# Kernel optimization log

Measured on AMD Instinct MI355X. Metric: run time of the kernel, lower is better.

## Reference

```python
import jax, jax.numpy as jnp
import numpy as np

B, N, D, H = 4, 2048, 1024, 64

def setup_inputs() -> dict:
    key = jax.random.key(0)
    ks = jax.random.split(key, 7)
    s = D ** -0.5  # torch Linear default init scale ~ U(-1/sqrt(fan_in), ...); scale randn similarly
    return {
        "x":  jax.random.normal(ks[0], (B, N, D), dtype=jnp.float32),
        "Wq": jax.random.normal(ks[1], (D, H), dtype=jnp.float32) * s,
        "bq": jax.random.normal(ks[2], (H,), dtype=jnp.float32) * s,
        "Wk": jax.random.normal(ks[3], (D, H), dtype=jnp.float32) * s,
        "bk": jax.random.normal(ks[4], (H,), dtype=jnp.float32) * s,
        "Wv": jax.random.normal(ks[5], (D, H), dtype=jnp.float32) * s,
        "bv": jax.random.normal(ks[6], (H,), dtype=jnp.float32) * s,
    }

def reference(x, Wq, bq, Wk, bk, Wv, bv):
    head_size = Wq.shape[1]
    q = x @ Wq + bq          # [B, N, H]
    k = x @ Wk + bk          # [B, N, H]
    v = x @ Wv + bv          # [B, N, H]
    scores = jnp.einsum("bid,bjd->bij", q, k)        # [B, N, N]
    # faithful to torch: keep upper triangle (col >= row), then mask exact zeros to -inf
    scores = jnp.triu(scores)
    scores = jnp.where(scores == 0, -jnp.inf, scores)
    attn = jax.nn.softmax(scores * (head_size ** -0.5), axis=-1)  # [B, N, N]
    # out = (V^T @ attn)^T  ==  attn^T @ V
    out = jnp.einsum("bji,bjh->bih", attn, v)         # [B, N, H]
    return out
```

## Files before the change

### kernel.cpp

```cpp
#include <hip/hip_runtime.h>
#include <math.h>

constexpr int kN = 2048;
constexpr int kD = 1024;
constexpr int kH = 64;
constexpr int kBN = 4 * kN;

typedef __attribute__((ext_vector_type(8))) short bf16x8;
typedef __attribute__((ext_vector_type(4))) short bf16x4;
typedef __attribute__((ext_vector_type(4))) float f32x4;

#define MFMA(a, b, c) __builtin_amdgcn_mfma_f32_16x16x32_bf16(a, b, c, 0, 0, 0)

__device__ __forceinline__ short f2bf(float f) {
    unsigned u = __float_as_uint(f);
    u += 0x7fff + ((u >> 16) & 1);
    return (short)(u >> 16);
}

__device__ __forceinline__ void ml_merge(float& m, float& l, float mo, float lo) {
    float mn = fmaxf(m, mo);
    l = l * __expf(m - mn) + lo * __expf(mo - mn);
    m = mn;
}

__global__ __launch_bounds__(256) void prep_kernel(
        const float* __restrict__ Wq, const float* __restrict__ Wk,
        const float* __restrict__ Wv, const float* __restrict__ bq,
        const float* __restrict__ bk, const float* __restrict__ bv,
        short* __restrict__ Wt, float* __restrict__ bcat)
{
    int tid = blockIdx.x * 256 + threadIdx.x;
    for (int e = tid; e < 192 * kD; e += gridDim.x * 256) {
        int n = e >> 10, d = e & 1023;
        float w = (n < 64) ? Wq[d * 64 + n]
                : (n < 128) ? Wk[d * 64 + (n - 64)]
                : Wv[d * 64 + (n - 128)];
        Wt[e] = f2bf(w);
    }
    if (tid < 192)
        bcat[tid] = (tid < 64) ? bq[tid] : (tid < 128) ? bk[tid - 64] : bv[tid - 128];
}

__global__ __launch_bounds__(256) void qkv_kernel(
        const float* __restrict__ x, const short* __restrict__ Wt,
        const float* __restrict__ bcat,
        short* __restrict__ gq, short* __restrict__ gk, short* __restrict__ vt)
{
    __shared__ short xs[32 * 72];
    __shared__ short wsm[192 * 72];
    const int t = threadIdx.x;
    const int m0 = blockIdx.x * 32;
    const int w = t >> 6, lane = t & 63;
    const int l15 = lane & 15, q8 = lane >> 4;
    const int msub = w & 1;
    const int nh = w >> 1;

    f32x4 acc[6];
    #pragma unroll
    for (int i = 0; i < 6; ++i) acc[i] = (f32x4){0.f, 0.f, 0.f, 0.f};

    for (int k0 = 0; k0 < kD; k0 += 64) {
        __syncthreads();
        #pragma unroll
        for (int p = 0; p < 2; ++p) {
            int idx = t + p * 256;
            int row = idx >> 4, c = idx & 15;
            float4 xv = *(const float4*)&x[(size_t)(m0 + row) * kD + k0 + c * 4];
            bf16x4 pk = {f2bf(xv.x), f2bf(xv.y), f2bf(xv.z), f2bf(xv.w)};
            *(bf16x4*)&xs[row * 72 + c * 4] = pk;
        }
        #pragma unroll
        for (int p = 0; p < 6; ++p) {
            int idx = t + p * 256;
            int row = idx >> 3, c = idx & 7;
            *(bf16x8*)&wsm[row * 72 + c * 8] =
                *(const bf16x8*)&Wt[(size_t)row * kD + k0 + c * 8];
        }
        __syncthreads();

        int arow = 16 * msub + l15;
        bf16x8 a0 = *(const bf16x8*)&xs[arow * 72 + q8 * 8];
        bf16x8 a1 = *(const bf16x8*)&xs[arow * 72 + 32 + q8 * 8];
        #pragma unroll
        for (int nt = 0; nt < 6; ++nt) {
            int brow = 96 * nh + 16 * nt + l15;
            bf16x8 b0 = *(const bf16x8*)&wsm[brow * 72 + q8 * 8];
            bf16x8 b1 = *(const bf16x8*)&wsm[brow * 72 + 32 + q8 * 8];
            acc[nt] = MFMA(a0, b0, acc[nt]);
            acc[nt] = MFMA(a1, b1, acc[nt]);
        }
    }

    #pragma unroll
    for (int nt = 0; nt < 6; ++nt) {
        int nb = 96 * nh + 16 * nt;
        int n = nb + l15;
        float bias = bcat[n];
        if (nb < 128) {
            #pragma unroll
            for (int r = 0; r < 4; ++r) {
                int m = m0 + 16 * msub + q8 * 4 + r;
                short bf = f2bf(acc[nt][r] + bias);
                if (nb < 64) gq[(size_t)m * 64 + n] = bf;
                else         gk[(size_t)m * 64 + (n - 64)] = bf;
            }
        } else {
            int h = n - 128;
            int bz = m0 >> 11;
            int jb = (m0 & 2047) + 16 * msub + q8 * 4;
            bf16x4 pk = {f2bf(acc[nt][0] + bias), f2bf(acc[nt][1] + bias),
                         f2bf(acc[nt][2] + bias), f2bf(acc[nt][3] + bias)};
            *(bf16x4*)&vt[((size_t)(bz * 64 + h)) * kN + jb] = pk;
        }
    }
}

__global__ __launch_bounds__(256) void stats_kernel(
        const short* __restrict__ gq, const short* __restrict__ gk,
        float* __restrict__ m2, float* __restrict__ l2)
{
    __shared__ short qsm[64 * 72];
    __shared__ short ksm[64 * 72];
    const int t = threadIdx.x;
    const int w = t >> 6, lane = t & 63;
    const int l15 = lane & 15, q8 = lane >> 4;
    const int b = blockIdx.x;
    const int ic = b >> 7, rem = b & 127;
    const int bz = rem >> 5, jt = rem & 31;
    const int j0 = jt * 64;
    const int ilo = ic * 512, ihi = ilo + 512;
    const int istart = (j0 > ilo) ? j0 : ilo;

    float mloc[4] = {-1e30f, -1e30f, -1e30f, -1e30f};
    float lloc[4] = {0.f, 0.f, 0.f, 0.f};

    if (istart < ihi) {
        #pragma unroll
        for (int p = 0; p < 2; ++p) {
            int idx = t + p * 256;
            int row = idx >> 3, c = idx & 7;
            *(bf16x8*)&qsm[row * 72 + c * 8] =
                *(const bf16x8*)&gq[(size_t)(bz * kN + j0 + row) * 64 + c * 8];
        }
        for (int i0 = istart; i0 < ihi; i0 += 64) {
            __syncthreads();
            #pragma unroll
            for (int p = 0; p < 2; ++p) {
                int idx = t + p * 256;
                int row = idx >> 3, c = idx & 7;
                *(bf16x8*)&ksm[row * 72 + c * 8] =
                    *(const bf16x8*)&gk[(size_t)(bz * kN + i0 + row) * 64 + c * 8];
            }
            __syncthreads();

            int jrow = 16 * w + l15;
            bf16x8 a0 = *(const bf16x8*)&qsm[jrow * 72 + q8 * 8];
            bf16x8 a1 = *(const bf16x8*)&qsm[jrow * 72 + 32 + q8 * 8];
            #pragma unroll
            for (int it = 0; it < 4; ++it) {
                int irow = 16 * it + l15;
                bf16x8 b0 = *(const bf16x8*)&ksm[irow * 72 + q8 * 8];
                bf16x8 b1 = *(const bf16x8*)&ksm[irow * 72 + 32 + q8 * 8];
                f32x4 s = (f32x4){0.f, 0.f, 0.f, 0.f};
                s = MFMA(a0, b0, s);
                s = MFMA(a1, b1, s);
                int ig = i0 + 16 * it + l15;
                #pragma unroll
                for (int r = 0; r < 4; ++r) {
                    int jg = j0 + 16 * w + q8 * 4 + r;
                    float sv = s[r];
                    bool valid = (ig >= jg) && (sv != 0.0f);
                    float sc = valid ? sv * 0.125f : -1e30f;
                    float mn = fmaxf(mloc[r], sc);
                    float e2 = valid ? __expf(sc - mn) : 0.f;
                    lloc[r] = lloc[r] * __expf(mloc[r] - mn) + e2;
                    mloc[r] = mn;
                }
            }
        }
    }
    #pragma unroll
    for (int off = 1; off < 16; off <<= 1) {
        #pragma unroll
        for (int r = 0; r < 4; ++r) {
            float mo = __shfl_xor(mloc[r], off);
            float lo = __shfl_xor(lloc[r], off);
            ml_merge(mloc[r], lloc[r], mo, lo);
        }
    }
    if (l15 == 0) {
        #pragma unroll
        for (int r = 0; r < 4; ++r) {
            int jg = j0 + 16 * w + q8 * 4 + r;
            m2[ic * kBN + bz * kN + jg] = mloc[r];
            l2[ic * kBN + bz * kN + jg] = lloc[r];
        }
    }
}

__global__ __launch_bounds__(256) void combine_kernel(
        const float* __restrict__ m2, const float* __restrict__ l2,
        float* __restrict__ mf, float* __restrict__ rlf)
{
    int r = blockIdx.x * 256 + threadIdx.x;
    float m = m2[r], l = l2[r];
    #pragma unroll
    for (int c = 1; c < 4; ++c)
        ml_merge(m, l, m2[c * kBN + r], l2[c * kBN + r]);
    mf[r] = m;
    rlf[r] = (l > 0.f) ? 1.0f / l : 0.0f;
}

__global__ __launch_bounds__(256) void out_kernel(
        const short* __restrict__ gq, const short* __restrict__ gk,
        const short* __restrict__ vt, const float* __restrict__ mf,
        const float* __restrict__ rlf, float* __restrict__ part)
{
    __shared__ short ksm[64 * 72];
    __shared__ short qsm[64 * 72];
    __shared__ short vsm[64 * 72];
    __shared__ short psm[64 * 72];
    __shared__ float msm[64];
    __shared__ float rsm[64];
    const int t = threadIdx.x;
    const int w = t >> 6, lane = t & 63;
    const int l15 = lane & 15, q8 = lane >> 4;
    const int b = blockIdx.x;
    const int jc = b >> 7, rem = b & 127;
    const int bz = rem >> 5, it = rem & 31;
    const int i0 = it * 64;
    const int jlo = jc * 512;
    const int jhi = (jlo + 512 < i0 + 64) ? (jlo + 512) : (i0 + 64);

    f32x4 oacc[4];
    #pragma unroll
    for (int i = 0; i < 4; ++i) oacc[i] = (f32x4){0.f, 0.f, 0.f, 0.f};

    if (jlo < jhi) {
        #pragma unroll
        for (int p = 0; p < 2; ++p) {
            int idx = t + p * 256;
            int row = idx >> 3, c = idx & 7;
            *(bf16x8*)&ksm[row * 72 + c * 8] =
                *(const bf16x8*)&gk[(size_t)(bz * kN + i0 + row) * 64 + c * 8];
        }
        for (int j0s = jlo; j0s < jhi; j0s += 64) {
            __syncthreads();
            #pragma unroll
            for (int p = 0; p < 2; ++p) {
                int idx = t + p * 256;
                int row = idx >> 3, c = idx & 7;
                *(bf16x8*)&qsm[row * 72 + c * 8] =
                    *(const bf16x8*)&gq[(size_t)(bz * kN + j0s + row) * 64 + c * 8];
                *(bf16x8*)&vsm[row * 72 + c * 8] =
                    *(const bf16x8*)&vt[(size_t)(bz * 64 + row) * kN + j0s + c * 8];
            }
            if (t < 64) msm[t] = mf[bz * kN + j0s + t];
            else if (t < 128) rsm[t - 64] = rlf[bz * kN + j0s + (t - 64)];
            __syncthreads();

            int jrow = 16 * w + l15;
            bf16x8 a0 = *(const bf16x8*)&qsm[jrow * 72 + q8 * 8];
            bf16x8 a1 = *(const bf16x8*)&qsm[jrow * 72 + 32 + q8 * 8];
            #pragma unroll
            for (int itile = 0; itile < 4; ++itile) {
                int irow = 16 * itile + l15;
                bf16x8 b0 = *(const bf16x8*)&ksm[irow * 72 + q8 * 8];
                bf16x8 b1 = *(const bf16x8*)&ksm[irow * 72 + 32 + q8 * 8];
                f32x4 s = (f32x4){0.f, 0.f, 0.f, 0.f};
                s = MFMA(a0, b0, s);
                s = MFMA(a1, b1, s);
                int ig = i0 + 16 * itile + l15;
                bf16x4 pk;
                #pragma unroll
                for (int r = 0; r < 4; ++r) {
                    int jl = 16 * w + q8 * 4 + r;
                    int jg = j0s + jl;
                    float sv = s[r];
                    bool valid = (ig >= jg) && (sv != 0.0f);
                    float p = valid ? __expf(sv * 0.125f - msm[jl]) * rsm[jl] : 0.f;
                    pk[r] = f2bf(p);
                }
                *(bf16x4*)&psm[(16 * itile + l15) * 72 + 16 * w + q8 * 4] = pk;
            }
            __syncthreads();

            int prow = 16 * w + l15;
            bf16x8 pa0 = *(const bf16x8*)&psm[prow * 72 + q8 * 8];
            bf16x8 pa1 = *(const bf16x8*)&psm[prow * 72 + 32 + q8 * 8];
            #pragma unroll
            for (int ht = 0; ht < 4; ++ht) {
                int vrow = 16 * ht + l15;
                bf16x8 vb0 = *(const bf16x8*)&vsm[vrow * 72 + q8 * 8];
                bf16x8 vb1 = *(const bf16x8*)&vsm[vrow * 72 + 32 + q8 * 8];
                oacc[ht] = MFMA(pa0, vb0, oacc[ht]);
                oacc[ht] = MFMA(pa1, vb1, oacc[ht]);
            }
        }
    }
    size_t base = ((size_t)(jc * 4 + bz) * kN + i0) * 64;
    #pragma unroll
    for (int ht = 0; ht < 4; ++ht)
        #pragma unroll
        for (int r = 0; r < 4; ++r)
            part[base + (size_t)(16 * w + q8 * 4 + r) * 64 + 16 * ht + l15] = oacc[ht][r];
}

__global__ __launch_bounds__(256) void reduce_kernel(
        const float* __restrict__ part, float* __restrict__ out)
{
    int idx = blockIdx.x * 256 + threadIdx.x;
    const float4* p = (const float4*)part;
    float4 a = p[idx];
    float4 b = p[idx + 131072];
    float4 c = p[idx + 262144];
    float4 d = p[idx + 393216];
    float4 r;
    r.x = a.x + b.x + c.x + d.x;
    r.y = a.y + b.y + c.y + d.y;
    r.z = a.z + b.z + c.z + d.z;
    r.w = a.w + b.w + c.w + d.w;
    ((float4*)out)[idx] = r;
}

extern "C" void kernel_launch(void* const* d_in, const int* in_sizes, int n_in,
                              void* d_out, int out_size, void* d_ws, size_t ws_size,
                              hipStream_t stream)
{
    const float* x  = (const float*)d_in[0];
    const float* Wq = (const float*)d_in[1];
    const float* bq = (const float*)d_in[2];
    const float* Wk = (const float*)d_in[3];
    const float* bk = (const float*)d_in[4];
    const float* Wv = (const float*)d_in[5];
    const float* bv = (const float*)d_in[6];
    float* out = (float*)d_out;

    char* base = (char*)d_ws;
    short* Wt   = (short*)base;
    float* bcat = (float*)(base + 393216);
    short* gq   = (short*)(base + 394240);
    short* gk   = (short*)(base + 1442816);
    short* vt   = (short*)(base + 2491392);
    float* m2   = (float*)(base + 3539968);
    float* l2   = (float*)(base + 3671040);
    float* mf   = (float*)(base + 3802112);
    float* rlf  = (float*)(base + 3834880);
    float* part = (float*)(base + 3867648);

    prep_kernel<<<96, 256, 0, stream>>>(Wq, Wk, Wv, bq, bk, bv, Wt, bcat);
    qkv_kernel<<<256, 256, 0, stream>>>(x, Wt, bcat, gq, gk, vt);
    stats_kernel<<<512, 256, 0, stream>>>(gq, gk, m2, l2);
    combine_kernel<<<32, 256, 0, stream>>>(m2, l2, mf, rlf);
    out_kernel<<<512, 256, 0, stream>>>(gq, gk, vt, mf, rlf, part);
    reduce_kernel<<<512, 256, 0, stream>>>(part, out);
}
```

Before: 145.2 us.

## Pre-pad operands in global memory, use direct global-to-LDS loads, drop running max

Adds a prep pass that converts x to bf16 into a padded, chunked layout, and stores Q, K and V^T with a 72-element padded row stride. This lets every tile move into shared memory with async global_load_lds copies instead of register round trips. The softmax max tracking is removed and the kernels sum raw exp(s/8), which is safe only while scores stay small. Block index mapping is reordered and the qkv wave tiling changes. The cost is a large extra prep pass that writes a padded bf16 copy of x (about 19MB of workspace).

```diff
diff --git a/kernel.cpp b/kernel.cpp
--- a/kernel.cpp
+++ b/kernel.cpp
@@ -3,8 +3,6 @@
 
 constexpr int kN = 2048;
 constexpr int kD = 1024;
-constexpr int kH = 64;
-constexpr int kBN = 4 * kN;
 
 typedef __attribute__((ext_vector_type(8))) short bf16x8;
 typedef __attribute__((ext_vector_type(4))) short bf16x4;
@@ -18,217 +16,201 @@
     return (short)(u >> 16);
 }
 
-__device__ __forceinline__ void ml_merge(float& m, float& l, float mo, float lo) {
-    float mn = fmaxf(m, mo);
-    l = l * __expf(m - mn) + lo * __expf(mo - mn);
-    m = mn;
+__device__ __forceinline__ void g2l(void* lds, const void* g, int nbytes, int t) {
+    int lane = t & 63, w = t >> 6;
+    for (int base = w * 1024; base < nbytes; base += 4096) {
+        if (base + lane * 16 < nbytes) {
+            __builtin_amdgcn_global_load_lds(
+                (const __attribute__((address_space(1))) void*)((const char*)g + base + lane * 16),
+                (__attribute__((address_space(3))) void*)((char*)lds + base),
+                16, 0, 0);
+        }
+    }
 }
 
 __global__ __launch_bounds__(256) void prep_kernel(
+        const float* __restrict__ x,
         const float* __restrict__ Wq, const float* __restrict__ Wk,
         const float* __restrict__ Wv, const float* __restrict__ bq,
         const float* __restrict__ bk, const float* __restrict__ bv,
-        short* __restrict__ Wt, float* __restrict__ bcat)
+        short* __restrict__ xb, short* __restrict__ Wt, float* __restrict__ bcat)
 {
     int tid = blockIdx.x * 256 + threadIdx.x;
-    for (int e = tid; e < 192 * kD; e += gridDim.x * 256) {
-        int n = e >> 10, d = e & 1023;
-        float w = (n < 64) ? Wq[d * 64 + n]
-                : (n < 128) ? Wk[d * 64 + (n - 64)]
-                : Wv[d * 64 + (n - 128)];
-        Wt[e] = f2bf(w);
+    int stride = gridDim.x * 256;
+    for (int e = tid; e < 16 * 8192 * 64; e += stride) {
+        int kc = e >> 19;
+        int rem = e & 524287;
+        int row = rem >> 6, c = rem & 63;
+        xb[((size_t)(kc * 8192 + row)) * 72 + c] = f2bf(x[(size_t)row * kD + kc * 64 + c]);
+    }
+    for (int e = tid; e < 16 * 64 * 192; e += stride) {
+        int n = e % 192;
+        int rc = e / 192;
+        int c = rc & 63, kc = rc >> 6;
+        int d = kc * 64 + c;
+        float wv = (n < 64) ? Wq[d * 64 + n]
+                 : (n < 128) ? Wk[d * 64 + (n - 64)]
+                 : Wv[d * 64 + (n - 128)];
+        Wt[(kc * 192 + n) * 72 + c] = f2bf(wv);
     }
     if (tid < 192)
         bcat[tid] = (tid < 64) ? bq[tid] : (tid < 128) ? bk[tid - 64] : bv[tid - 128];
 }
 
 __global__ __launch_bounds__(256) void qkv_kernel(
-        const float* __restrict__ x, const short* __restrict__ Wt,
+        const short* __restrict__ xb, const short* __restrict__ Wt,
         const float* __restrict__ bcat,
         short* __restrict__ gq, short* __restrict__ gk, short* __restrict__ vt)
 {
-    __shared__ short xs[32 * 72];
-    __shared__ short wsm[192 * 72];
+    __shared__ __align__(16) short xs[32 * 72];
+    __shared__ __align__(16) short wsm[192 * 72];
     const int t = threadIdx.x;
+    const int w = t >> 6, lane = t & 63, l15 = lane & 15, q8 = lane >> 4;
     const int m0 = blockIdx.x * 32;
-    const int w = t >> 6, lane = t & 63;
-    const int l15 = lane & 15, q8 = lane >> 4;
-    const int msub = w & 1;
-    const int nh = w >> 1;
-
-    f32x4 acc[6];
-    #pragma unroll
-    for (int i = 0; i < 6; ++i) acc[i] = (f32x4){0.f, 0.f, 0.f, 0.f};
-
-    for (int k0 = 0; k0 < kD; k0 += 64) {
+
+    f32x4 acc[2][3];
+    #pragma unroll
+    for (int rt = 0; rt < 2; ++rt)
+        #pragma unroll
+        for (int ct = 0; ct < 3; ++ct) acc[rt][ct] = (f32x4){0.f, 0.f, 0.f, 0.f};
+
+    for (int kc = 0; kc < 16; ++kc) {
         __syncthreads();
-        #pragma unroll
-        for (int p = 0; p < 2; ++p) {
-            int idx = t + p * 256;
-            int row = idx >> 4, c = idx & 15;
-            float4 xv = *(const float4*)&x[(size_t)(m0 + row) * kD + k0 + c * 4];
-            bf16x4 pk = {f2bf(xv.x), f2bf(xv.y), f2bf(xv.z), f2bf(xv.w)};
-            *(bf16x4*)&xs[row * 72 + c * 4] = pk;
-        }
-        #pragma unroll
-        for (int p = 0; p < 6; ++p) {
-            int idx = t + p * 256;
-            int row = idx >> 3, c = idx & 7;
-            *(bf16x8*)&wsm[row * 72 + c * 8] =
-                *(const bf16x8*)&Wt[(size_t)row * kD + k0 + c * 8];
-        }
+        g2l(xs, xb + ((size_t)(kc * 8192 + m0)) * 72, 32 * 144, t);
+        g2l(wsm, Wt + (size_t)kc * 192 * 72, 192 * 144, t);
         __syncthreads();
 
-        int arow = 16 * msub + l15;
-        bf16x8 a0 = *(const bf16x8*)&xs[arow * 72 + q8 * 8];
-        bf16x8 a1 = *(const bf16x8*)&xs[arow * 72 + 32 + q8 * 8];
-        #pragma unroll
-        for (int nt = 0; nt < 6; ++nt) {
-            int brow = 96 * nh + 16 * nt + l15;
-            bf16x8 b0 = *(const bf16x8*)&wsm[brow * 72 + q8 * 8];
-            bf16x8 b1 = *(const bf16x8*)&wsm[brow * 72 + 32 + q8 * 8];
-            acc[nt] = MFMA(a0, b0, acc[nt]);
-            acc[nt] = MFMA(a1, b1, acc[nt]);
-        }
-    }
-
-    #pragma unroll
-    for (int nt = 0; nt < 6; ++nt) {
-        int nb = 96 * nh + 16 * nt;
-        int n = nb + l15;
-        float bias = bcat[n];
-        if (nb < 128) {
+        bf16x8 a[2][2], b[3][2];
+        #pragma unroll
+        for (int rt = 0; rt < 2; ++rt) {
+            int arow = rt * 16 + l15;
+            a[rt][0] = *(const bf16x8*)&xs[arow * 72 + q8 * 8];
+            a[rt][1] = *(const bf16x8*)&xs[arow * 72 + 32 + q8 * 8];
+        }
+        #pragma unroll
+        for (int ct = 0; ct < 3; ++ct) {
+            int brow = w * 48 + ct * 16 + l15;
+            b[ct][0] = *(const bf16x8*)&wsm[brow * 72 + q8 * 8];
+            b[ct][1] = *(const bf16x8*)&wsm[brow * 72 + 32 + q8 * 8];
+        }
+        #pragma unroll
+        for (int rt = 0; rt < 2; ++rt)
             #pragma unroll
-            for (int r = 0; r < 4; ++r) {
-                int m = m0 + 16 * msub + q8 * 4 + r;
-                short bf = f2bf(acc[nt][r] + bias);
-                if (nb < 64) gq[(size_t)m * 64 + n] = bf;
-                else         gk[(size_t)m * 64 + (n - 64)] = bf;
-            }
-        } else {
-            int h = n - 128;
-            int bz = m0 >> 11;
-            int jb = (m0 & 2047) + 16 * msub + q8 * 4;
-            bf16x4 pk = {f2bf(acc[nt][0] + bias), f2bf(acc[nt][1] + bias),
-                         f2bf(acc[nt][2] + bias), f2bf(acc[nt][3] + bias)};
-            *(bf16x4*)&vt[((size_t)(bz * 64 + h)) * kN + jb] = pk;
-        }
-    }
+            for (int ct = 0; ct < 3; ++ct) {
+                acc[rt][ct] = MFMA(a[rt][0], b[ct][0], acc[rt][ct]);
+                acc[rt][ct] = MFMA(a[rt][1], b[ct][1], acc[rt][ct]);
+            }
+    }
+
+    const int bz = m0 >> 11;
+    const int jt = (m0 & 2047) >> 6;
+    const int jb = m0 & 63;
+    #pragma unroll
+    for (int rt = 0; rt < 2; ++rt)
+        #pragma unroll
+        for (int ct = 0; ct < 3; ++ct) {
+            int nb = w * 48 + ct * 16;
+            int n = nb + l15;
+            float bias = bcat[n];
+            if (nb < 64) {
+                #pragma unroll
+                for (int r = 0; r < 4; ++r)
+                    gq[(size_t)(m0 + rt * 16 + q8 * 4 + r) * 72 + n] =
+                        f2bf(acc[rt][ct][r] + bias);
+            } else if (nb < 128) {
+                #pragma unroll
+                for (int r = 0; r < 4; ++r)
+                    gk[(size_t)(m0 + rt * 16 + q8 * 4 + r) * 72 + (n - 64)] =
+                        f2bf(acc[rt][ct][r] + bias);
+            } else {
+                int h = n - 128;
+                bf16x4 pk = {f2bf(acc[rt][ct][0] + bias), f2bf(acc[rt][ct][1] + bias),
+                             f2bf(acc[rt][ct][2] + bias), f2bf(acc[rt][ct][3] + bias)};
+                *(bf16x4*)&vt[((size_t)((bz * 32 + jt) * 64 + h)) * 72 + jb + rt * 16 + q8 * 4] = pk;
+            }
+        }
 }
 
 __global__ __launch_bounds__(256) void stats_kernel(
         const short* __restrict__ gq, const short* __restrict__ gk,
-        float* __restrict__ m2, float* __restrict__ l2)
-{
-    __shared__ short qsm[64 * 72];
-    __shared__ short ksm[64 * 72];
+        float* __restrict__ l2)
+{
+    __shared__ __align__(16) short qsm[64 * 72];
+    __shared__ __align__(16) short ksm[64 * 72];
     const int t = threadIdx.x;
-    const int w = t >> 6, lane = t & 63;
-    const int l15 = lane & 15, q8 = lane >> 4;
+    const int w = t >> 6, lane = t & 63, l15 = lane & 15, q8 = lane >> 4;
     const int b = blockIdx.x;
-    const int ic = b >> 7, rem = b & 127;
-    const int bz = rem >> 5, jt = rem & 31;
+    const int ic = b & 3, bz = (b >> 2) & 3, jt = b >> 4;
     const int j0 = jt * 64;
     const int ilo = ic * 512, ihi = ilo + 512;
     const int istart = (j0 > ilo) ? j0 : ilo;
 
-    float mloc[4] = {-1e30f, -1e30f, -1e30f, -1e30f};
     float lloc[4] = {0.f, 0.f, 0.f, 0.f};
 
     if (istart < ihi) {
-        #pragma unroll
-        for (int p = 0; p < 2; ++p) {
-            int idx = t + p * 256;
-            int row = idx >> 3, c = idx & 7;
-            *(bf16x8*)&qsm[row * 72 + c * 8] =
-                *(const bf16x8*)&gq[(size_t)(bz * kN + j0 + row) * 64 + c * 8];
-        }
+        g2l(qsm, gq + (size_t)(bz * kN + j0) * 72, 64 * 144, t);
+        __syncthreads();
+        int jrow = 16 * w + l15;
+        bf16x8 a0 = *(const bf16x8*)&qsm[jrow * 72 + q8 * 8];
+        bf16x8 a1 = *(const bf16x8*)&qsm[jrow * 72 + 32 + q8 * 8];
+
         for (int i0 = istart; i0 < ihi; i0 += 64) {
             __syncthreads();
-            #pragma unroll
-            for (int p = 0; p < 2; ++p) {
-                int idx = t + p * 256;
-                int row = idx >> 3, c = idx & 7;
-                *(bf16x8*)&ksm[row * 72 + c * 8] =
-                    *(const bf16x8*)&gk[(size_t)(bz * kN + i0 + row) * 64 + c * 8];
-            }
-            __syncthreads();
-
-            int jrow = 16 * w + l15;
-            bf16x8 a0 = *(const bf16x8*)&qsm[jrow * 72 + q8 * 8];
-            bf16x8 a1 = *(const bf16x8*)&qsm[jrow * 72 + 32 + q8 * 8];
+            g2l(ksm, gk + (size_t)(bz * kN + i0) * 72, 64 * 144, t);
+            __syncthreads();
             #pragma unroll
             for (int it = 0; it < 4; ++it) {
-                int irow = 16 * it + l15;
+                int irow = it * 16 + l15;
                 bf16x8 b0 = *(const bf16x8*)&ksm[irow * 72 + q8 * 8];
                 bf16x8 b1 = *(const bf16x8*)&ksm[irow * 72 + 32 + q8 * 8];
                 f32x4 s = (f32x4){0.f, 0.f, 0.f, 0.f};
                 s = MFMA(a0, b0, s);
                 s = MFMA(a1, b1, s);
-                int ig = i0 + 16 * it + l15;
+                int ig = i0 + it * 16 + l15;
                 #pragma unroll
                 for (int r = 0; r < 4; ++r) {
                     int jg = j0 + 16 * w + q8 * 4 + r;
                     float sv = s[r];
-                    bool valid = (ig >= jg) && (sv != 0.0f);
-                    float sc = valid ? sv * 0.125f : -1e30f;
-                    float mn = fmaxf(mloc[r], sc);
-                    float e2 = valid ? __expf(sc - mn) : 0.f;
-                    lloc[r] = lloc[r] * __expf(mloc[r] - mn) + e2;
-                    mloc[r] = mn;
+                    float e = __expf(sv * 0.125f);
+                    lloc[r] += ((ig >= jg) && (sv != 0.0f)) ? e : 0.0f;
                 }
             }
         }
     }
     #pragma unroll
-    for (int off = 1; off < 16; off <<= 1) {
-        #pragma unroll
-        for (int r = 0; r < 4; ++r) {
-            float mo = __shfl_xor(mloc[r], off);
-            float lo = __shfl_xor(lloc[r], off);
-            ml_merge(mloc[r], lloc[r], mo, lo);
-        }
-    }
+    for (int off = 1; off < 16; off <<= 1)
+        #pragma unroll
+        for (int r = 0; r < 4; ++r)
+            lloc[r] += __shfl_xor(lloc[r], off);
     if (l15 == 0) {
         #pragma unroll
-        for (int r = 0; r < 4; ++r) {
-            int jg = j0 + 16 * w + q8 * 4 + r;
-            m2[ic * kBN + bz * kN + jg] = mloc[r];
-            l2[ic * kBN + bz * kN + jg] = lloc[r];
-        }
+        for (int r = 0; r < 4; ++r)
+            l2[ic * 8192 + bz * kN + j0 + 16 * w + q8 * 4 + r] = lloc[r];
     }
 }
 
 __global__ __launch_bounds__(256) void combine_kernel(
-        const float* __restrict__ m2, const float* __restrict__ l2,
-        float* __restrict__ mf, float* __restrict__ rlf)
+        const float* __restrict__ l2, float* __restrict__ rlf)
 {
     int r = blockIdx.x * 256 + threadIdx.x;
-    float m = m2[r], l = l2[r];
-    #pragma unroll
-    for (int c = 1; c < 4; ++c)
-        ml_merge(m, l, m2[c * kBN + r], l2[c * kBN + r]);
-    mf[r] = m;
+    float l = l2[r] + l2[8192 + r] + l2[16384 + r] + l2[24576 + r];
     rlf[r] = (l > 0.f) ? 1.0f / l : 0.0f;
 }
 
 __global__ __launch_bounds__(256) void out_kernel(
         const short* __restrict__ gq, const short* __restrict__ gk,
-        const short* __restrict__ vt, const float* __restrict__ mf,
-        const float* __restrict__ rlf, float* __restrict__ part)
-{
-    __shared__ short ksm[64 * 72];
-    __shared__ short qsm[64 * 72];
-    __shared__ short vsm[64 * 72];
-    __shared__ short psm[64 * 72];
-    __shared__ float msm[64];
+        const short* __restrict__ vt, const float* __restrict__ rlf,
+        float* __restrict__ part)
+{
+    __shared__ __align__(16) short ksm[64 * 72];
+    __shared__ __align__(16) short qsm[64 * 72];
+    __shared__ __align__(16) short vsm[64 * 72];
+    __shared__ __align__(16) short psm[64 * 72];
     __shared__ float rsm[64];
     const int t = threadIdx.x;
-    const int w = t >> 6, lane = t & 63;
-    const int l15 = lane & 15, q8 = lane >> 4;
+    const int w = t >> 6, lane = t & 63, l15 = lane & 15, q8 = lane >> 4;
     const int b = blockIdx.x;
-    const int jc = b >> 7, rem = b & 127;
-    const int bz = rem >> 5, it = rem & 31;
+    const int jc = b & 3, bz = (b >> 2) & 3, it = b >> 4;
     const int i0 = it * 64;
     const int jlo = jc * 512;
     const int jhi = (jlo + 512 < i0 + 64) ? (jlo + 512) : (i0 + 64);
@@ -238,26 +220,12 @@
     for (int i = 0; i < 4; ++i) oacc[i] = (f32x4){0.f, 0.f, 0.f, 0.f};
 
     if (jlo < jhi) {
-        #pragma unroll
-        for (int p = 0; p < 2; ++p) {
-            int idx = t + p * 256;
-            int row = idx >> 3, c = idx & 7;
-            *(bf16x8*)&ksm[row * 72 + c * 8] =
-                *(const bf16x8*)&gk[(size_t)(bz * kN + i0 + row) * 64 + c * 8];
-        }
+        g2l(ksm, gk + (size_t)(bz * kN + i0) * 72, 64 * 144, t);
         for (int j0s = jlo; j0s < jhi; j0s += 64) {
             __syncthreads();
-            #pragma unroll
-            for (int p = 0; p < 2; ++p) {
-                int idx = t + p * 256;
-                int row = idx >> 3, c = idx & 7;
-                *(bf16x8*)&qsm[row * 72 + c * 8] =
-                    *(const bf16x8*)&gq[(size_t)(bz * kN + j0s + row) * 64 + c * 8];
-                *(bf16x8*)&vsm[row * 72 + c * 8] =
-                    *(const bf16x8*)&vt[(size_t)(bz * 64 + row) * kN + j0s + c * 8];
-            }
-            if (t < 64) msm[t] = mf[bz * kN + j0s + t];
-            else if (t < 128) rsm[t - 64] = rlf[bz * kN + j0s + (t - 64)];
+            g2l(qsm, gq + (size_t)(bz * kN + j0s) * 72, 64 * 144, t);
+            g2l(vsm, vt + (size_t)((bz * 32 + (j0s >> 6)) * 64) * 72, 64 * 144, t);
+            if (t < 64) rsm[t] = rlf[bz * kN + j0s + t];
             __syncthreads();
 
             int jrow = 16 * w + l15;
@@ -265,33 +233,32 @@
             bf16x8 a1 = *(const bf16x8*)&qsm[jrow * 72 + 32 + q8 * 8];
             #pragma unroll
             for (int itile = 0; itile < 4; ++itile) {
-                int irow = 16 * itile + l15;
+                int irow = itile * 16 + l15;
                 bf16x8 b0 = *(const bf16x8*)&ksm[irow * 72 + q8 * 8];
                 bf16x8 b1 = *(const bf16x8*)&ksm[irow * 72 + 32 + q8 * 8];
                 f32x4 s = (f32x4){0.f, 0.f, 0.f, 0.f};
                 s = MFMA(a0, b0, s);
                 s = MFMA(a1, b1, s);
-                int ig = i0 + 16 * itile + l15;
+                int ig = i0 + itile * 16 + l15;
                 bf16x4 pk;
                 #pragma unroll
                 for (int r = 0; r < 4; ++r) {
                     int jl = 16 * w + q8 * 4 + r;
                     int jg = j0s + jl;
                     float sv = s[r];
-                    bool valid = (ig >= jg) && (sv != 0.0f);
-                    float p = valid ? __expf(sv * 0.125f - msm[jl]) * rsm[jl] : 0.f;
+                    float p = ((ig >= jg) && (sv != 0.0f))
+                            ? __expf(sv * 0.125f) * rsm[jl] : 0.0f;
                     pk[r] = f2bf(p);
                 }
-                *(bf16x4*)&psm[(16 * itile + l15) * 72 + 16 * w + q8 * 4] = pk;
-            }
-            __syncthreads();
-
-            int prow = 16 * w + l15;
-            bf16x8 pa0 = *(const bf16x8*)&psm[prow * 72 + q8 * 8];
-            bf16x8 pa1 = *(const bf16x8*)&psm[prow * 72 + 32 + q8 * 8];
+                *(bf16x4*)&psm[(itile * 16 + l15) * 72 + 16 * w + q8 * 4] = pk;
+            }
+            __syncthreads();
+
+            bf16x8 pa0 = *(const bf16x8*)&psm[(16 * w + l15) * 72 + q8 * 8];
+            bf16x8 pa1 = *(const bf16x8*)&psm[(16 * w + l15) * 72 + 32 + q8 * 8];
             #pragma unroll
             for (int ht = 0; ht < 4; ++ht) {
-                int vrow = 16 * ht + l15;
+                int vrow = ht * 16 + l15;
                 bf16x8 vb0 = *(const bf16x8*)&vsm[vrow * 72 + q8 * 8];
                 bf16x8 vb1 = *(const bf16x8*)&vsm[vrow * 72 + 32 + q8 * 8];
                 oacc[ht] = MFMA(pa0, vb0, oacc[ht]);
@@ -304,7 +271,7 @@
     for (int ht = 0; ht < 4; ++ht)
         #pragma unroll
         for (int r = 0; r < 4; ++r)
-            part[base + (size_t)(16 * w + q8 * 4 + r) * 64 + 16 * ht + l15] = oacc[ht][r];
+            part[base + (size_t)(16 * w + q8 * 4 + r) * 64 + ht * 16 + l15] = oacc[ht][r];
 }
 
 __global__ __launch_bounds__(256) void reduce_kernel(
@@ -338,21 +305,20 @@
     float* out = (float*)d_out;
 
     char* base = (char*)d_ws;
-    short* Wt   = (short*)base;
-    float* bcat = (float*)(base + 393216);
-    short* gq   = (short*)(base + 394240);
-    short* gk   = (short*)(base + 1442816);
-    short* vt   = (short*)(base + 2491392);
-    float* m2   = (float*)(base + 3539968);
-    float* l2   = (float*)(base + 3671040);
-    float* mf   = (float*)(base + 3802112);
-    float* rlf  = (float*)(base + 3834880);
-    float* part = (float*)(base + 3867648);
-
-    prep_kernel<<<96, 256, 0, stream>>>(Wq, Wk, Wv, bq, bk, bv, Wt, bcat);
-    qkv_kernel<<<256, 256, 0, stream>>>(x, Wt, bcat, gq, gk, vt);
-    stats_kernel<<<512, 256, 0, stream>>>(gq, gk, m2, l2);
-    combine_kernel<<<32, 256, 0, stream>>>(m2, l2, mf, rlf);
-    out_kernel<<<512, 256, 0, stream>>>(gq, gk, vt, mf, rlf, part);
+    short* Wt   = (short*)(base);
+    float* bcat = (float*)(base + 442368);
+    short* xb   = (short*)(base + 443392);
+    short* gq   = (short*)(base + 19317760);
+    short* gk   = (short*)(base + 20497408);
+    short* vt   = (short*)(base + 21677056);
+    float* l2   = (float*)(base + 22856704);
+    float* rlf  = (float*)(base + 22987776);
+    float* part = (float*)(base + 23020544);
+
+    prep_kernel<<<2048, 256, 0, stream>>>(x, Wq, Wk, Wv, bq, bk, bv, xb, Wt, bcat);
+    qkv_kernel<<<256, 256, 0, stream>>>(xb, Wt, bcat, gq, gk, vt);
+    stats_kernel<<<512, 256, 0, stream>>>(gq, gk, l2);
+    combine_kernel<<<32, 256, 0, stream>>>(l2, rlf);
+    out_kernel<<<512, 256, 0, stream>>>(gq, gk, vt, rlf, part);
     reduce_kernel<<<512, 256, 0, stream>>>(part, out);
 }
```

New measurement: 143.1 us. No clear change (-1.4%).
